# Optimization experiments

Measured on AMD Instinct MI355X. Metric: run time of the kernel, lower is better.

Reference implementation:

```python
import jax, jax.numpy as jnp
import numpy as np

LN_EPS = 1e-5  # torch.nn.LayerNorm default

QLEN, MLEN, BATCH, D_MODEL = 1024, 1024, 8, 1024


def _ft_matrix(qlen, klen):
    """Real part of the causal Fourier matrix (imag part never contributes:
    the input is real and the module takes .real of the product)."""
    ft_len = klen - qlen + 1
    m = jnp.arange(qlen, dtype=jnp.float32)
    k = jnp.arange(ft_len, dtype=jnp.float32)
    base = jnp.cos((2.0 * float(np.pi)) * jnp.outer(m, k) / float(ft_len))
    base = base / float(np.sqrt(ft_len))                      # [qlen, ft_len]
    mat = jnp.pad(base, ((0, 0), (klen - ft_len, 0)))          # left-pad -> [qlen, klen]
    # row i rolled left by (qlen - 1 - i), vectorized as a gather
    shift = (qlen - 1) - jnp.arange(qlen)                      # [qlen]
    cols = (jnp.arange(klen)[None, :] + shift[:, None]) % klen  # [qlen, klen]
    mat = jnp.take_along_axis(mat, cols, axis=1)
    rows = jnp.arange(qlen)[:, None]
    js = jnp.arange(klen)[None, :]
    # tril(diagonal=klen-qlen) AND triu(0)  (same_length=True)
    mask = (js <= rows + (klen - qlen)) & (js >= rows)
    return jnp.where(mask, mat, jnp.float32(0.0))


def setup_inputs() -> dict:
    key = jax.random.key(0)
    k1, k2, k3 = jax.random.split(key, 3)
    return {
        "dec_inp": jax.random.normal(k1, (QLEN, BATCH, D_MODEL), dtype=jnp.float32),
        "pos_emb": jax.random.normal(k2, (QLEN + MLEN, 1, D_MODEL), dtype=jnp.float32),
        "mems": jax.random.normal(k3, (MLEN, BATCH, D_MODEL), dtype=jnp.float32),
        "gamma": jnp.ones((D_MODEL,), dtype=jnp.float32),
        "beta": jnp.zeros((D_MODEL,), dtype=jnp.float32),
        "add_position": 1,
    }


def reference(dec_inp, pos_emb, mems, gamma, beta, add_position):
    qlen = dec_inp.shape[0]
    klen = qlen + mems.shape[0]
    cat = jnp.concatenate([mems, dec_inp], axis=0)  # [klen, b, d]
    if add_position:
        cat = cat + pos_emb  # dropout is identity in eval mode
    ft_mat = _ft_matrix(qlen, klen)                 # [qlen, klen]
    ft = jnp.einsum('ml,lbd->mbd', ft_mat, cat)     # real part of complex matmul
    x = dec_inp + ft / float(np.sqrt(klen))
    mu = jnp.mean(x, axis=-1, keepdims=True)
    var = jnp.var(x, axis=-1, keepdims=True)
    return gamma * (x - mu) * jax.lax.rsqrt(var + LN_EPS) + beta
```

## Files before the change

kernel.cpp:

```cpp
#include <hip/hip_runtime.h>
#include <hip/hip_bf16.h>

#define QLEN   1024
#define MLEN   1024
#define KLEN   2048
#define BATCH  8
#define DMODEL 1024
#define NCOLS  (BATCH * DMODEL)
#define FTLEN  1025

typedef __attribute__((ext_vector_type(4))) float f32x4;
typedef __attribute__((ext_vector_type(8))) short bf16x8;

typedef __attribute__((address_space(1))) const unsigned int as1_u32;
typedef __attribute__((address_space(3))) unsigned int as3_u32;

static __device__ __forceinline__ unsigned short f2bf(float f) {
    unsigned int u = __builtin_bit_cast(unsigned int, f);
    return (unsigned short)((u + 0x7fffu + ((u >> 16) & 1u)) >> 16);
}

__global__ __launch_bounds__(256) void prep_transpose(
    const float* __restrict__ dec, const float* __restrict__ pos,
    const float* __restrict__ mems, const int* __restrict__ addp,
    unsigned short* __restrict__ catT)
{
    __shared__ unsigned short T[64][72];
    const int lt = blockIdx.x, dt = blockIdx.y, b = blockIdx.z;
    const int tid = threadIdx.x;
    const int add_position = addp[0];
    const int l0 = lt * 64, d0 = dt * 64;

    const int lrow = tid >> 4;
    const int dcol = (tid & 15) * 4;
    for (int p = 0; p < 4; ++p) {
        const int ll = p * 16 + lrow;
        const int l = l0 + ll;
        const int d = d0 + dcol;
        const float* src = (l < MLEN)
            ? (mems + (size_t)l * NCOLS + b * DMODEL + d)
            : (dec + (size_t)(l - MLEN) * NCOLS + b * DMODEL + d);
        float4 v = *reinterpret_cast<const float4*>(src);
        if (add_position) {
            float4 pv = *reinterpret_cast<const float4*>(pos + (size_t)l * DMODEL + d);
            v.x += pv.x; v.y += pv.y; v.z += pv.z; v.w += pv.w;
        }
        T[dcol + 0][ll] = f2bf(v.x);
        T[dcol + 1][ll] = f2bf(v.y);
        T[dcol + 2][ll] = f2bf(v.z);
        T[dcol + 3][ll] = f2bf(v.w);
    }
    __syncthreads();
    for (int p = 0; p < 2; ++p) {
        const int idx = p * 256 + tid;
        const int r = idx >> 3;
        const int c = (idx & 7) * 8;
        int4 v = *reinterpret_cast<const int4*>(&T[r][c]);
        size_t n = (size_t)(b * DMODEL + d0 + r);
        *reinterpret_cast<int4*>(&catT[n * KLEN + l0 + c]) = v;
    }
}

__global__ __launch_bounds__(256) void fill_w(unsigned short* __restrict__ W)
{
    const int idx = blockIdx.x * 256 + threadIdx.x;
    const int m = idx >> 9;
    const int k4 = (idx & 511) * 4;
    union { unsigned short s[4]; int2 v; } u;
    for (int j = 0; j < 4; ++j) {
        const int k = k4 + j;
        const int t = k - m;
        float w = 0.0f;
        if (t >= 0 && t < FTLEN) {
            const int r = (m * t) % FTLEN;
            const float theta = (6.283185307179586f / (float)FTLEN) * (float)r;
            w = cosf(theta) * 0.03123475237772121f;
        }
        u.s[j] = f2bf(w);
    }
    *reinterpret_cast<int2*>(&W[(size_t)m * KLEN + k4]) = u.v;
}

__global__ __launch_bounds__(256) void gemm_band(
    const unsigned short* __restrict__ W,
    const unsigned short* __restrict__ catT,
    const float* __restrict__ dec,
    float* __restrict__ xout)
{
    __shared__ unsigned short Alds[128 * 64];
    __shared__ unsigned short Blds[128 * 64];
    const int tid = threadIdx.x;
    const int wave = tid >> 6, lane = tid & 63;
    const int m0 = blockIdx.x * 128;
    const int n0 = blockIdx.y * 128;
    const int wm = wave >> 1, wn = wave & 1;

    f32x4 acc[4][4];
    for (int i = 0; i < 4; ++i)
        for (int j = 0; j < 4; ++j)
            acc[i][j] = (f32x4){0.f, 0.f, 0.f, 0.f};

    const int srow = lane >> 3;
    const int scol = (lane & 7) * 8;
    const int fr = lane & 15;
    const int kg = lane >> 4;

    for (int t = 0; t < 18; ++t) {
        const int k0 = m0 + t * 64;
        for (int i = 0; i < 4; ++i) {
            const int row = (i * 4 + wave) * 8 + srow;
            __builtin_amdgcn_global_load_lds(
                (as1_u32*)(const void*)(W + (size_t)(m0 + row) * KLEN + k0 + scol),
                (as3_u32*)(void*)(Alds + row * 64 + scol), 16, 0, 0);
            __builtin_amdgcn_global_load_lds(
                (as1_u32*)(const void*)(catT + (size_t)(n0 + row) * KLEN + k0 + scol),
                (as3_u32*)(void*)(Blds + row * 64 + scol), 16, 0, 0);
        }
        __syncthreads();

        for (int ks = 0; ks < 2; ++ks) {
            bf16x8 a[4], b[4];
            for (int f = 0; f < 4; ++f) {
                a[f] = *reinterpret_cast<const bf16x8*>(
                    Alds + (wm * 64 + f * 16 + fr) * 64 + ks * 32 + kg * 8);
                b[f] = *reinterpret_cast<const bf16x8*>(
                    Blds + (wn * 64 + f * 16 + fr) * 64 + ks * 32 + kg * 8);
            }
            for (int fm = 0; fm < 4; ++fm)
                for (int fn = 0; fn < 4; ++fn)
                    acc[fm][fn] = __builtin_amdgcn_mfma_f32_16x16x32_bf16(
                        a[fm], b[fn], acc[fm][fn], 0, 0, 0);
        }
        __syncthreads();
    }

    const float inv = 0.022097086912079612f;
    const int col16 = lane & 15, rquad = lane >> 4;
    for (int fm = 0; fm < 4; ++fm)
        for (int fn = 0; fn < 4; ++fn)
            for (int j = 0; j < 4; ++j) {
                const int m = m0 + wm * 64 + fm * 16 + rquad * 4 + j;
                const int n = n0 + wn * 64 + fn * 16 + col16;
                const size_t o = (size_t)m * NCOLS + n;
                xout[o] = dec[o] + acc[fm][fn][j] * inv;
            }
}

__global__ __launch_bounds__(256) void layernorm_rows(
    const float* __restrict__ x, const float* __restrict__ gamma,
    const float* __restrict__ beta, float* __restrict__ out)
{
    __shared__ float ps[4], pq[4];
    const int row = blockIdx.x;
    const int tid = threadIdx.x;
    const float* xr = x + (size_t)row * DMODEL;
    float4 v = *reinterpret_cast<const float4*>(xr + tid * 4);
    float s  = v.x + v.y + v.z + v.w;
    float sq = v.x * v.x + v.y * v.y + v.z * v.z + v.w * v.w;
    for (int off = 32; off > 0; off >>= 1) {
        s  += __shfl_down(s, off);
        sq += __shfl_down(sq, off);
    }
    const int wave = tid >> 6, lane = tid & 63;
    if (lane == 0) { ps[wave] = s; pq[wave] = sq; }
    __syncthreads();
    if (tid == 0) {
        float ts = ps[0] + ps[1] + ps[2] + ps[3];
        float tq = pq[0] + pq[1] + pq[2] + pq[3];
        float mu = ts * (1.0f / DMODEL);
        float var = tq * (1.0f / DMODEL) - mu * mu;
        ps[0] = mu;
        pq[0] = rsqrtf(var + 1e-5f);
    }
    __syncthreads();
    const float mu = ps[0], rs = pq[0];
    float4 g  = *reinterpret_cast<const float4*>(gamma + tid * 4);
    float4 be = *reinterpret_cast<const float4*>(beta + tid * 4);
    float4 o;
    o.x = g.x * (v.x - mu) * rs + be.x;
    o.y = g.y * (v.y - mu) * rs + be.y;
    o.z = g.z * (v.z - mu) * rs + be.z;
    o.w = g.w * (v.w - mu) * rs + be.w;
    *reinterpret_cast<float4*>(out + (size_t)row * DMODEL + tid * 4) = o;
}

extern "C" void kernel_launch(void* const* d_in, const int* in_sizes, int n_in,
                              void* d_out, int out_size, void* d_ws, size_t ws_size,
                              hipStream_t stream)
{
    const float* dec   = (const float*)d_in[0];
    const float* pos   = (const float*)d_in[1];
    const float* mems  = (const float*)d_in[2];
    const float* gamma = (const float*)d_in[3];
    const float* beta  = (const float*)d_in[4];
    const int*   addp  = (const int*)d_in[5];
    float* out = (float*)d_out;

    unsigned short* catT = (unsigned short*)d_ws;
    unsigned short* Wmat = catT + (size_t)NCOLS * KLEN;
    float* x = (float*)(Wmat + (size_t)QLEN * KLEN);

    prep_transpose<<<dim3(32, 16, 8), 256, 0, stream>>>(dec, pos, mems, addp, catT);
    fill_w<<<2048, 256, 0, stream>>>(Wmat);
    gemm_band<<<dim3(8, 64), 256, 0, stream>>>(Wmat, catT, dec, x);
    layernorm_rows<<<8192, 256, 0, stream>>>(x, gamma, beta, out);
}
```

Before: 74.45 us.

## Triple-buffer banded GEMM with larger tiles, XCD-aware mapping, bf16 intermediate

Replaces the 128x128 single-buffered GEMM with a 128x256 tile, 512-thread kernel. It uses a three-stage LDS ring with async global-to-LDS loads prefetched two steps ahead and explicit vmcnt waits, and a block index remap that groups N tiles per XCD. The pre-layernorm intermediate is now stored as bf16 instead of fp32, which halves that write and read traffic. The cost is extra rounding before the layernorm statistics and higher LDS use per block, which limits occupancy.

```diff
diff --git a/kernel.cpp b/kernel.cpp
--- a/kernel.cpp
+++ b/kernel.cpp
@@ -9,6 +9,11 @@
 #define NCOLS  (BATCH * DMODEL)
 #define FTLEN  1025
 
+#define BM 128
+#define BN 256
+#define BK 64
+#define NT 18
+
 typedef __attribute__((ext_vector_type(4))) float f32x4;
 typedef __attribute__((ext_vector_type(8))) short bf16x8;
 
@@ -18,6 +23,9 @@
 static __device__ __forceinline__ unsigned short f2bf(float f) {
     unsigned int u = __builtin_bit_cast(unsigned int, f);
     return (unsigned short)((u + 0x7fffu + ((u >> 16) & 1u)) >> 16);
+}
+static __device__ __forceinline__ float bf2f(unsigned short s) {
+    return __builtin_bit_cast(float, (unsigned int)s << 16);
 }
 
 __global__ __launch_bounds__(256) void prep_transpose(
@@ -81,82 +89,117 @@
     *reinterpret_cast<int2*>(&W[(size_t)m * KLEN + k4]) = u.v;
 }
 
-__global__ __launch_bounds__(256) void gemm_band(
+__global__ __launch_bounds__(512) void gemm_band2(
     const unsigned short* __restrict__ W,
     const unsigned short* __restrict__ catT,
     const float* __restrict__ dec,
-    float* __restrict__ xout)
-{
-    __shared__ unsigned short Alds[128 * 64];
-    __shared__ unsigned short Blds[128 * 64];
+    unsigned short* __restrict__ xout)
+{
+    __shared__ unsigned short Alds[3][BM * BK];
+    __shared__ unsigned short Blds[3][BN * BK];
+
     const int tid = threadIdx.x;
     const int wave = tid >> 6, lane = tid & 63;
-    const int m0 = blockIdx.x * 128;
-    const int n0 = blockIdx.y * 128;
-    const int wm = wave >> 1, wn = wave & 1;
+
+    const int bid = blockIdx.x;
+    const int xcd = bid & 7;
+    const int kk = bid >> 3;
+    const int m_idx = kk >> 2;
+    const int n_idx = xcd * 4 + (kk & 3);
+    const int m0 = m_idx * BM, n0 = n_idx * BN;
+    const int wm = wave >> 2, wn = wave & 3;
 
     f32x4 acc[4][4];
     for (int i = 0; i < 4; ++i)
         for (int j = 0; j < 4; ++j)
             acc[i][j] = (f32x4){0.f, 0.f, 0.f, 0.f};
 
-    const int srow = lane >> 3;
-    const int scol = (lane & 7) * 8;
+    const int srow = tid >> 3;
+    const int scol = (tid & 7) * 8;
     const int fr = lane & 15;
     const int kg = lane >> 4;
 
-    for (int t = 0; t < 18; ++t) {
-        const int k0 = m0 + t * 64;
-        for (int i = 0; i < 4; ++i) {
-            const int row = (i * 4 + wave) * 8 + srow;
-            __builtin_amdgcn_global_load_lds(
-                (as1_u32*)(const void*)(W + (size_t)(m0 + row) * KLEN + k0 + scol),
-                (as3_u32*)(void*)(Alds + row * 64 + scol), 16, 0, 0);
-            __builtin_amdgcn_global_load_lds(
-                (as1_u32*)(const void*)(catT + (size_t)(n0 + row) * KLEN + k0 + scol),
-                (as3_u32*)(void*)(Blds + row * 64 + scol), 16, 0, 0);
-        }
-        __syncthreads();
-
+#define STAGE(S, T) do {                                                        \
+    const int k0_ = m0 + (T) * BK;                                              \
+    _Pragma("unroll")                                                           \
+    for (int p = 0; p < 2; ++p) {                                               \
+        const int row = p * 64 + srow;                                          \
+        __builtin_amdgcn_global_load_lds(                                       \
+            (as1_u32*)(const void*)(W + (size_t)(m0 + row) * KLEN + k0_ + scol),\
+            (as3_u32*)(void*)(&Alds[S][row * BK + scol]), 16, 0, 0);            \
+    }                                                                           \
+    _Pragma("unroll")                                                           \
+    for (int p = 0; p < 4; ++p) {                                               \
+        const int row = p * 64 + srow;                                          \
+        __builtin_amdgcn_global_load_lds(                                       \
+            (as1_u32*)(const void*)(catT + (size_t)(n0 + row) * KLEN + k0_ + scol),\
+            (as3_u32*)(void*)(&Blds[S][row * BK + scol]), 16, 0, 0);            \
+    }                                                                           \
+} while (0)
+
+    STAGE(0, 0);
+    STAGE(1, 1);
+
+    for (int t = 0; t < NT; ++t) {
+        if (t == NT - 1)
+            asm volatile("s_waitcnt vmcnt(0)\ns_barrier" ::: "memory");
+        else
+            asm volatile("s_waitcnt vmcnt(6)\ns_barrier" ::: "memory");
+
+        if (t + 2 < NT) {
+            const int s = (t + 2) % 3;
+            STAGE(s, t + 2);
+        }
+
+        const unsigned short* Ab = Alds[t % 3];
+        const unsigned short* Bb = Blds[t % 3];
+#pragma unroll
         for (int ks = 0; ks < 2; ++ks) {
             bf16x8 a[4], b[4];
-            for (int f = 0; f < 4; ++f) {
+#pragma unroll
+            for (int f = 0; f < 4; ++f)
                 a[f] = *reinterpret_cast<const bf16x8*>(
-                    Alds + (wm * 64 + f * 16 + fr) * 64 + ks * 32 + kg * 8);
+                    Ab + (wm * 64 + f * 16 + fr) * BK + ks * 32 + kg * 8);
+#pragma unroll
+            for (int f = 0; f < 4; ++f)
                 b[f] = *reinterpret_cast<const bf16x8*>(
-                    Blds + (wn * 64 + f * 16 + fr) * 64 + ks * 32 + kg * 8);
-            }
+                    Bb + (wn * 64 + f * 16 + fr) * BK + ks * 32 + kg * 8);
+#pragma unroll
             for (int fm = 0; fm < 4; ++fm)
+#pragma unroll
                 for (int fn = 0; fn < 4; ++fn)
                     acc[fm][fn] = __builtin_amdgcn_mfma_f32_16x16x32_bf16(
                         a[fm], b[fn], acc[fm][fn], 0, 0, 0);
         }
-        __syncthreads();
-    }
+    }
+#undef STAGE
 
     const float inv = 0.022097086912079612f;
     const int col16 = lane & 15, rquad = lane >> 4;
+#pragma unroll
     for (int fm = 0; fm < 4; ++fm)
+#pragma unroll
         for (int fn = 0; fn < 4; ++fn)
+#pragma unroll
             for (int j = 0; j < 4; ++j) {
                 const int m = m0 + wm * 64 + fm * 16 + rquad * 4 + j;
                 const int n = n0 + wn * 64 + fn * 16 + col16;
                 const size_t o = (size_t)m * NCOLS + n;
-                xout[o] = dec[o] + acc[fm][fn][j] * inv;
+                xout[o] = f2bf(dec[o] + acc[fm][fn][j] * inv);
             }
 }
 
 __global__ __launch_bounds__(256) void layernorm_rows(
-    const float* __restrict__ x, const float* __restrict__ gamma,
+    const unsigned short* __restrict__ x, const float* __restrict__ gamma,
     const float* __restrict__ beta, float* __restrict__ out)
 {
     __shared__ float ps[4], pq[4];
     const int row = blockIdx.x;
     const int tid = threadIdx.x;
-    const float* xr = x + (size_t)row * DMODEL;
-    float4 v = *reinterpret_cast<const float4*>(xr + tid * 4);
-    float s  = v.x + v.y + v.z + v.w;
-    float sq = v.x * v.x + v.y * v.y + v.z * v.z + v.w * v.w;
+    ushort4 u = *reinterpret_cast<const ushort4*>(x + (size_t)row * DMODEL + tid * 4);
+    float vx = bf2f(u.x), vy = bf2f(u.y), vz = bf2f(u.z), vw = bf2f(u.w);
+    float s  = vx + vy + vz + vw;
+    float sq = vx * vx + vy * vy + vz * vz + vw * vw;
     for (int off = 32; off > 0; off >>= 1) {
         s  += __shfl_down(s, off);
         sq += __shfl_down(sq, off);
@@ -177,10 +220,10 @@
     float4 g  = *reinterpret_cast<const float4*>(gamma + tid * 4);
     float4 be = *reinterpret_cast<const float4*>(beta + tid * 4);
     float4 o;
-    o.x = g.x * (v.x - mu) * rs + be.x;
-    o.y = g.y * (v.y - mu) * rs + be.y;
-    o.z = g.z * (v.z - mu) * rs + be.z;
-    o.w = g.w * (v.w - mu) * rs + be.w;
+    o.x = g.x * (vx - mu) * rs + be.x;
+    o.y = g.y * (vy - mu) * rs + be.y;
+    o.z = g.z * (vz - mu) * rs + be.z;
+    o.w = g.w * (vw - mu) * rs + be.w;
     *reinterpret_cast<float4*>(out + (size_t)row * DMODEL + tid * 4) = o;
 }
 
@@ -198,10 +241,10 @@
 
     unsigned short* catT = (unsigned short*)d_ws;
     unsigned short* Wmat = catT + (size_t)NCOLS * KLEN;
-    float* x = (float*)(Wmat + (size_t)QLEN * KLEN);
+    unsigned short* x    = Wmat + (size_t)QLEN * KLEN;
 
     prep_transpose<<<dim3(32, 16, 8), 256, 0, stream>>>(dec, pos, mems, addp, catT);
     fill_w<<<2048, 256, 0, stream>>>(Wmat);
-    gemm_band<<<dim3(8, 64), 256, 0, stream>>>(Wmat, catT, dec, x);
+    gemm_band2<<<256, 512, 0, stream>>>(Wmat, catT, dec, x);
     layernorm_rows<<<8192, 256, 0, stream>>>(x, gamma, beta, out);
 }
```

New measurement: 76.45 us. 1.03x slower.
